# Kernel tuning notes

Hardware: AMD Instinct MI355X
Metric: run time of the kernel (lower is better)

The kernel has to match this reference:

```python
import jax, jax.numpy as jnp
import numpy as np
import math

D_MODEL = 1024
N_HEADS = 16
D_K = D_MODEL // N_HEADS
WIDTH_MULTIPLIER = 1.0  # readout=False on all projections, so unused in math


def setup_inputs() -> dict:
    key = jax.random.key(0)
    kx, kq, kk, kv, ko = jax.random.split(key, 5)
    std = 1.0 / math.sqrt(D_MODEL)  # init_scale=1.0 / sqrt(in_features)
    x = jax.random.normal(kx, (2, 2048, D_MODEL), dtype=jnp.float32)
    # weights stored as (out_features, in_features), matching torch
    Wq = jax.random.normal(kq, (D_MODEL, D_MODEL), dtype=jnp.float32) * std
    Wk = jax.random.normal(kk, (D_MODEL, D_MODEL), dtype=jnp.float32) * std
    Wv = jax.random.normal(kv, (D_MODEL, D_MODEL), dtype=jnp.float32) * std
    Wo = jax.random.normal(ko, (D_MODEL, D_MODEL), dtype=jnp.float32) * std
    return {"x": x, "Wq": Wq, "Wk": Wk, "Wv": Wv, "Wo": Wo}


def reference(x, Wq, Wk, Wv, Wo):
    B, S, D = x.shape
    H, Dk = N_HEADS, D_K
    # muPLinear: x @ W.T (bias=False, readout=False)
    q = jnp.einsum('bsd,ed->bse', x, Wq).reshape(B, S, H, Dk).transpose(0, 2, 1, 3)
    k = jnp.einsum('bsd,ed->bse', x, Wk).reshape(B, S, H, Dk).transpose(0, 2, 1, 3)
    v = jnp.einsum('bsd,ed->bse', x, Wv).reshape(B, S, H, Dk).transpose(0, 2, 1, 3)
    # full [B,H,S,S] scores, scaled by 1/sqrt(d_k), softmax over keys
    scores = jnp.einsum('bhqd,bhkd->bhqk', q, k) / math.sqrt(Dk)
    attn = jax.nn.softmax(scores, axis=-1)
    out = jnp.einsum('bhqk,bhkd->bhqd', attn, v)
    out = out.transpose(0, 2, 1, 3).reshape(B, S, D)
    return jnp.einsum('bsd,ed->bse', out, Wo)
```

## Files before the change

kernel.cpp:

```cpp
#include <hip/hip_runtime.h>
#include <hip/hip_bf16.h>
#include <math.h>

#define D_MODEL 1024
#define N_HEADS 16
#define D_K     64
#define BATCH   2
#define SEQ     2048
#define M_TOTAL (BATCH * SEQ)

typedef __attribute__((ext_vector_type(8))) short short8;
typedef __attribute__((ext_vector_type(4))) float f32x4;
typedef __attribute__((ext_vector_type(16))) float f32x16;

__device__ __forceinline__ ushort f2bf(float f) {
    __hip_bfloat16 h = __float2bfloat16(f);
    union { __hip_bfloat16 h; ushort u; } c; c.h = h; return c.u;
}

__device__ __forceinline__ uint packbf(float a, float b) {
    return ((uint)f2bf(b) << 16) | (uint)f2bf(a);
}

__device__ __forceinline__ void gload_lds16(const void* g, void* l) {
    __builtin_amdgcn_global_load_lds(
        (const __attribute__((address_space(1))) void*)g,
        (__attribute__((address_space(3))) void*)l, 16, 0, 0);
}

__device__ __forceinline__ void plswap(uint& a, uint& b) {
    asm volatile("v_permlane32_swap_b32 %0, %1" : "+v"(a), "+v"(b));
}

__global__ __launch_bounds__(256) void cast_all(const float* __restrict__ x,
                                                const float* __restrict__ Wq,
                                                const float* __restrict__ Wk,
                                                const float* __restrict__ Wv,
                                                const float* __restrict__ Wo,
                                                ushort* __restrict__ xb,
                                                ushort* __restrict__ wqkv,
                                                ushort* __restrict__ wob)
{
    const int bi = blockIdx.x;
    const float* src; ushort* dst; int blk;
    const int NW = D_MODEL * D_MODEL;
    if (bi < 4096)      { src = x;  dst = xb;            blk = bi; }
    else if (bi < 5120) { src = Wq; dst = wqkv;          blk = bi - 4096; }
    else if (bi < 6144) { src = Wk; dst = wqkv + NW;     blk = bi - 5120; }
    else if (bi < 7168) { src = Wv; dst = wqkv + 2 * NW; blk = bi - 6144; }
    else                { src = Wo; dst = wob;           blk = bi - 7168; }
    const int i = blk * 1024 + threadIdx.x * 4;
    float4 v = *(const float4*)&src[i];
    ushort4 o;
    o.x = f2bf(v.x); o.y = f2bf(v.y); o.z = f2bf(v.z); o.w = f2bf(v.w);
    *(ushort4*)&dst[i] = o;
}

template <int EPI>
__global__ __launch_bounds__(256) void gemm_bf16(const ushort* __restrict__ A,
                                                 const ushort* __restrict__ B,
                                                 void* __restrict__ C0,
                                                 void* __restrict__ C1,
                                                 void* __restrict__ C2,
                                                 int M, int N, int K)
{
    __shared__ ushort As[2][4 * 128 * 8];
    __shared__ ushort Bs[2][4 * 128 * 8];

    const int tid = threadIdx.x;
    const int lane = tid & 63;
    const int w = tid >> 6;
    const int li = lane & 15;
    const int kg = lane >> 4;
    const int m0 = blockIdx.y * 128;
    const int n0 = blockIdx.x * 128;
    const int wr = (w >> 1) * 64;
    const int wc = (w & 1) * 64;

    f32x4 acc[4][4] = {};

    const int s1 = tid, s2 = tid + 256;
    const ushort* ga1 = &A[(size_t)(m0 + (s1 & 127)) * K + (s1 >> 7) * 8];
    const ushort* ga2 = &A[(size_t)(m0 + (s2 & 127)) * K + (s2 >> 7) * 8];
    const ushort* gb1 = &B[(size_t)(n0 + (s1 & 127)) * K + (s1 >> 7) * 8];
    const ushort* gb2 = &B[(size_t)(n0 + (s2 & 127)) * K + (s2 >> 7) * 8];

    const int NT = K / 32;
    gload_lds16(ga1, &As[0][s1 * 8]);
    gload_lds16(ga2, &As[0][s2 * 8]);
    gload_lds16(gb1, &Bs[0][s1 * 8]);
    gload_lds16(gb2, &Bs[0][s2 * 8]);

    for (int t = 0; t < NT; ++t) {
        const int cur = t & 1;
        asm volatile("s_waitcnt vmcnt(0)" ::: "memory");
        __syncthreads();
        if (t + 1 < NT) {
            const int kb = (t + 1) * 32;
            const int nxt = cur ^ 1;
            gload_lds16(ga1 + kb, &As[nxt][s1 * 8]);
            gload_lds16(ga2 + kb, &As[nxt][s2 * 8]);
            gload_lds16(gb1 + kb, &Bs[nxt][s1 * 8]);
            gload_lds16(gb2 + kb, &Bs[nxt][s2 * 8]);
        }
        short8 af[4], bf_[4];
#pragma unroll
        for (int m = 0; m < 4; ++m)
            af[m] = *(const short8*)&As[cur][(kg * 128 + wr + m * 16 + li) * 8];
#pragma unroll
        for (int n = 0; n < 4; ++n)
            bf_[n] = *(const short8*)&Bs[cur][(kg * 128 + wc + n * 16 + li) * 8];
#pragma unroll
        for (int m = 0; m < 4; ++m)
#pragma unroll
            for (int n = 0; n < 4; ++n)
                acc[m][n] = __builtin_amdgcn_mfma_f32_16x16x32_bf16(
                    af[m], bf_[n], acc[m][n], 0, 0, 0);
    }

    if (EPI == 1) {
        ushort* q = (ushort*)C0; ushort* k = (ushort*)C1; ushort* v = (ushort*)C2;
        const float QSCALE = 0.125f * 1.44269504088896f;
#pragma unroll
        for (int m = 0; m < 4; ++m) {
            const int Rb = m0 + wr + m * 16 + kg * 4;
#pragma unroll
            for (int n = 0; n < 4; ++n) {
                const int Ncol = n0 + wc + n * 16 + li;
                const int proj = Ncol >> 10;
                const int rem = Ncol & 1023;
                const int h = rem >> 6, dk = rem & 63;
#pragma unroll
                for (int r = 0; r < 4; ++r) {
                    const int R = Rb + r;
                    const int b = R >> 11, s = R & 2047;
                    const int bh = b * N_HEADS + h;
                    if (proj == 0)
                        q[((size_t)bh * SEQ + s) * D_K + dk] = f2bf(acc[m][n][r] * QSCALE);
                    else if (proj == 1)
                        k[((size_t)bh * SEQ + s) * D_K + dk] = f2bf(acc[m][n][r]);
                    else
                        v[((size_t)bh * D_K + dk) * SEQ + s] = f2bf(acc[m][n][r]);
                }
            }
        }
    } else {
        float* C = (float*)C0;
#pragma unroll
        for (int m = 0; m < 4; ++m) {
            const int Rb = m0 + wr + m * 16 + kg * 4;
#pragma unroll
            for (int n = 0; n < 4; ++n) {
                const int Ncol = n0 + wc + n * 16 + li;
#pragma unroll
                for (int r = 0; r < 4; ++r)
                    C[(size_t)(Rb + r) * N + Ncol] = acc[m][n][r];
            }
        }
    }
}

__global__ __launch_bounds__(256) void attn_mfma(const ushort* __restrict__ Q,
                                                 const ushort* __restrict__ K,
                                                 const ushort* __restrict__ Vt,
                                                 ushort* __restrict__ AO)
{
    __shared__ ushort Ks[2][64 * 64];
    __shared__ ushort Vs[2][64 * 64];

    const int tid = threadIdx.x, lane = tid & 63, w = tid >> 6;
    const int r31 = lane & 31, hi = lane >> 5;
    const int b = blockIdx.z, h = blockIdx.y, q0 = blockIdx.x * 128;
    const int bh = b * N_HEADS + h;
    const size_t base = (size_t)bh * SEQ * D_K;
    const size_t vbase = (size_t)bh * D_K * SEQ;

    uint pa = (uint)lane, pbv = 1000u + (uint)lane;
    plswap(pa, pbv);
    const bool swap_lo = (__builtin_amdgcn_readfirstlane(pa) > 500u);

    const size_t qrow = base + (size_t)(q0 + w * 32 + r31) * D_K;
    short8 qb[4];
#pragma unroll
    for (int ks = 0; ks < 4; ++ks)
        qb[ks] = *(const short8*)&Q[qrow + ks * 16 + hi * 8];

    float m_ = -INFINITY, l_ = 0.f;
    f32x16 o0 = {}, o1 = {};

    const int srow_l = lane >> 3;
    const int sblk = lane & 7;
    const ushort* Kt0 = &K[base];
    const ushort* Vt0 = &Vt[vbase];

#define STAGE(kt_, buf_)                                                      \
    {                                                                         \
        _Pragma("unroll")                                                     \
        for (int p = 0; p < 2; ++p) {                                         \
            const int row = w * 16 + p * 8 + srow_l;                          \
            const int db = sblk ^ (row & 7);                                  \
            gload_lds16(Kt0 + ((size_t)((kt_) * 64 + row)) * D_K + db * 8,    \
                        &Ks[buf_][(w * 16 + p * 8) * 64]);                    \
            gload_lds16(Vt0 + (size_t)row * SEQ + (kt_) * 64 + db * 8,        \
                        &Vs[buf_][(w * 16 + p * 8) * 64]);                    \
        }                                                                     \
    }

    STAGE(0, 0);

    const int NT = SEQ / 64;
    for (int kt = 0; kt < NT; ++kt) {
        const int cur = kt & 1;
        asm volatile("s_waitcnt vmcnt(0)" ::: "memory");
        __syncthreads();
        if (kt + 1 < NT) STAGE(kt + 1, cur ^ 1);

        f32x16 s0 = {}, s1 = {};
#pragma unroll
        for (int ks = 0; ks < 4; ++ks) {
            const int row = r31;
            short8 kb = *(const short8*)&Ks[cur][row * 64 + (((2 * ks + hi) ^ (row & 7)) * 8)];
            s0 = __builtin_amdgcn_mfma_f32_32x32x16_bf16(kb, qb[ks], s0, 0, 0, 0);
        }
#pragma unroll
        for (int ks = 0; ks < 4; ++ks) {
            const int row = 32 + r31;
            short8 kb = *(const short8*)&Ks[cur][row * 64 + (((2 * ks + hi) ^ (row & 7)) * 8)];
            s1 = __builtin_amdgcn_mfma_f32_32x32x16_bf16(kb, qb[ks], s1, 0, 0, 0);
        }

        float mx = fmaxf(s0[0], s0[1]);
#pragma unroll
        for (int e = 2; e < 16; ++e) mx = fmaxf(mx, s0[e]);
#pragma unroll
        for (int e = 0; e < 16; ++e) mx = fmaxf(mx, s1[e]);
        mx = fmaxf(mx, __shfl_xor(mx, 32, 64));

        if (__any(mx > m_ + 8.0f)) {
            const float mn = fmaxf(m_, mx);
            const float sc = exp2f(m_ - mn);
            l_ *= sc;
#pragma unroll
            for (int e = 0; e < 16; ++e) { o0[e] *= sc; o1[e] *= sc; }
            m_ = mn;
        }

        f32x16 p0, p1;
        float ts = 0.f;
#pragma unroll
        for (int e = 0; e < 16; ++e) { p0[e] = exp2f(s0[e] - m_); ts += p0[e]; }
#pragma unroll
        for (int e = 0; e < 16; ++e) { p1[e] = exp2f(s1[e] - m_); ts += p1[e]; }
        ts += __shfl_xor(ts, 32, 64);
        l_ += ts;

        uint u[8][2];
#pragma unroll
        for (int rq = 0; rq < 4; ++rq) {
            u[rq][0]     = packbf(p0[4 * rq + 0], p0[4 * rq + 1]);
            u[rq][1]     = packbf(p0[4 * rq + 2], p0[4 * rq + 3]);
            u[4 + rq][0] = packbf(p1[4 * rq + 0], p1[4 * rq + 1]);
            u[4 + rq][1] = packbf(p1[4 * rq + 2], p1[4 * rq + 3]);
        }

        short8 pb[4];
#pragma unroll
        for (int ks = 0; ks < 4; ++ks) {
            uint x0 = u[2 * ks][0], x1 = u[2 * ks][1];
            uint y0 = u[2 * ks + 1][0], y1 = u[2 * ks + 1][1];
            if (swap_lo) { plswap(y0, x0); plswap(y1, x1); }
            else         { plswap(x0, y0); plswap(x1, y1); }
            union { uint u4[4]; short8 s; } pu;
            pu.u4[0] = x0; pu.u4[1] = x1; pu.u4[2] = y0; pu.u4[3] = y1;
            pb[ks] = pu.s;
        }

#pragma unroll
        for (int ks = 0; ks < 4; ++ks) {
            const int row = r31;
            short8 vb = *(const short8*)&Vs[cur][row * 64 + (((2 * ks + hi) ^ (row & 7)) * 8)];
            o0 = __builtin_amdgcn_mfma_f32_32x32x16_bf16(vb, pb[ks], o0, 0, 0, 0);
        }
#pragma unroll
        for (int ks = 0; ks < 4; ++ks) {
            const int row = 32 + r31;
            short8 vb = *(const short8*)&Vs[cur][row * 64 + (((2 * ks + hi) ^ (row & 7)) * 8)];
            o1 = __builtin_amdgcn_mfma_f32_32x32x16_bf16(vb, pb[ks], o1, 0, 0, 0);
        }
    }
#undef STAGE

    const float inv = 1.0f / l_;
    ushort* Ao = &AO[((size_t)b * SEQ + q0 + w * 32 + r31) * D_MODEL + h * 64];
#pragma unroll
    for (int rq = 0; rq < 4; ++rq) {
        uint2 v0, v1;
        v0.x = packbf(o0[4 * rq + 0] * inv, o0[4 * rq + 1] * inv);
        v0.y = packbf(o0[4 * rq + 2] * inv, o0[4 * rq + 3] * inv);
        v1.x = packbf(o1[4 * rq + 0] * inv, o1[4 * rq + 1] * inv);
        v1.y = packbf(o1[4 * rq + 2] * inv, o1[4 * rq + 3] * inv);
        *(uint2*)&Ao[8 * rq + 4 * hi]      = v0;
        *(uint2*)&Ao[32 + 8 * rq + 4 * hi] = v1;
    }
}

extern "C" void kernel_launch(void* const* d_in, const int* in_sizes, int n_in,
                              void* d_out, int out_size, void* d_ws, size_t ws_size,
                              hipStream_t stream)
{
    const float* x  = (const float*)d_in[0];
    const float* Wq = (const float*)d_in[1];
    const float* Wk = (const float*)d_in[2];
    const float* Wv = (const float*)d_in[3];
    const float* Wo = (const float*)d_in[4];
    float* out = (float*)d_out;

    ushort* xb   = (ushort*)d_ws;
    ushort* Wqkv = xb + (size_t)M_TOTAL * D_MODEL;
    ushort* Wob  = Wqkv + (size_t)3 * D_MODEL * D_MODEL;
    ushort* q    = Wob + (size_t)D_MODEL * D_MODEL;
    ushort* k    = q + (size_t)M_TOTAL * D_MODEL;
    ushort* vt   = k + (size_t)M_TOTAL * D_MODEL;
    ushort* ao   = vt + (size_t)M_TOTAL * D_MODEL;

    hipLaunchKernelGGL(cast_all, dim3(8192), dim3(256), 0, stream,
                       x, Wq, Wk, Wv, Wo, xb, Wqkv, Wob);

    hipLaunchKernelGGL((gemm_bf16<1>), dim3(3 * D_MODEL / 128, M_TOTAL / 128), dim3(256),
                       0, stream, xb, Wqkv, q, k, vt, M_TOTAL, 3 * D_MODEL, D_MODEL);

    hipLaunchKernelGGL(attn_mfma, dim3(SEQ / 128, N_HEADS, BATCH), dim3(256),
                       0, stream, q, k, vt, ao);

    hipLaunchKernelGGL((gemm_bf16<0>), dim3(D_MODEL / 128, M_TOTAL / 128), dim3(256),
                       0, stream, ao, Wob, out, (void*)0, (void*)0,
                       M_TOTAL, D_MODEL, D_MODEL);
}
```

Baseline: 187.5 us.

## Split attention KV range across two wave groups per block and merge in LDS

The attention block now has 512 threads. Two groups of four waves each process half of the key/value sequence for the same 128 query rows, each group with its own double-buffered LDS tiles. The partial softmax states (m, l, O) are then merged through shared memory before the output is written. The change also precomputes the swizzled LDS offsets, wraps the MFMA sections in s_setprio, and replaces the software bf16 packing with the v_cvt_pk_bf16_f32 instruction. The aim is to double the waves per tile and the memory-level parallelism, since the grid of 512 blocks would otherwise leave the GPU underfilled, at the cost of more LDS and an extra merge step.

```diff
diff --git a/kernel.cpp b/kernel.cpp
--- a/kernel.cpp
+++ b/kernel.cpp
@@ -20,6 +20,12 @@
 
 __device__ __forceinline__ uint packbf(float a, float b) {
     return ((uint)f2bf(b) << 16) | (uint)f2bf(a);
+}
+
+__device__ __forceinline__ uint cvtpk(float a, float b) {
+    uint r;
+    asm("v_cvt_pk_bf16_f32 %0, %1, %2" : "=v"(r) : "v"(a), "v"(b));
+    return r;
 }
 
 __device__ __forceinline__ void gload_lds16(const void* g, void* l) {
@@ -160,15 +166,15 @@
     }
 }
 
-__global__ __launch_bounds__(256) void attn_mfma(const ushort* __restrict__ Q,
-                                                 const ushort* __restrict__ K,
-                                                 const ushort* __restrict__ Vt,
-                                                 ushort* __restrict__ AO)
+__global__ __launch_bounds__(512, 4) void attn_mfma(const ushort* __restrict__ Q,
+                                                    const ushort* __restrict__ K,
+                                                    const ushort* __restrict__ Vt,
+                                                    ushort* __restrict__ AO)
 {
-    __shared__ ushort Ks[2][64 * 64];
-    __shared__ ushort Vs[2][64 * 64];
+    __shared__ ushort pool[2][2][2][64 * 64];
 
     const int tid = threadIdx.x, lane = tid & 63, w = tid >> 6;
+    const int wq = w & 3, kvh = w >> 2;
     const int r31 = lane & 31, hi = lane >> 5;
     const int b = blockIdx.z, h = blockIdx.y, q0 = blockIdx.x * 128;
     const int bh = b * N_HEADS + h;
@@ -179,7 +185,7 @@
     plswap(pa, pbv);
     const bool swap_lo = (__builtin_amdgcn_readfirstlane(pa) > 500u);
 
-    const size_t qrow = base + (size_t)(q0 + w * 32 + r31) * D_K;
+    const size_t qrow = base + (size_t)(q0 + wq * 32 + r31) * D_K;
     short8 qb[4];
 #pragma unroll
     for (int ks = 0; ks < 4; ++ks)
@@ -192,42 +198,55 @@
     const int sblk = lane & 7;
     const ushort* Kt0 = &K[base];
     const ushort* Vt0 = &Vt[vbase];
-
-#define STAGE(kt_, buf_)                                                      \
-    {                                                                         \
-        _Pragma("unroll")                                                     \
-        for (int p = 0; p < 2; ++p) {                                         \
-            const int row = w * 16 + p * 8 + srow_l;                          \
-            const int db = sblk ^ (row & 7);                                  \
-            gload_lds16(Kt0 + ((size_t)((kt_) * 64 + row)) * D_K + db * 8,    \
-                        &Ks[buf_][(w * 16 + p * 8) * 64]);                    \
-            gload_lds16(Vt0 + (size_t)row * SEQ + (kt_) * 64 + db * 8,        \
-                        &Vs[buf_][(w * 16 + p * 8) * 64]);                    \
-        }                                                                     \
+    const int tile0 = kvh * 16;
+
+    const int xr = r31 & 7;
+    int off[2][4];
+#pragma unroll
+    for (int hf = 0; hf < 2; ++hf)
+#pragma unroll
+        for (int ks = 0; ks < 4; ++ks)
+            off[hf][ks] = hf * 2048 + r31 * 64 + (((2 * ks + hi) ^ xr) * 8);
+
+    const ushort* Kst = &pool[kvh][0][0][0];
+    const ushort* Vst = &pool[kvh][1][0][0];
+
+#define STAGE(kt_, buf_)                                                       \
+    {                                                                          \
+        _Pragma("unroll")                                                      \
+        for (int p = 0; p < 2; ++p) {                                          \
+            const int row = wq * 16 + p * 8 + srow_l;                          \
+            const int db = sblk ^ (row & 7);                                   \
+            gload_lds16(Kt0 + ((size_t)((tile0 + (kt_)) * 64 + row)) * D_K + db * 8, \
+                        &pool[kvh][0][buf_][(wq * 16 + p * 8) * 64]);          \
+            gload_lds16(Vt0 + (size_t)row * SEQ + (tile0 + (kt_)) * 64 + db * 8,     \
+                        &pool[kvh][1][buf_][(wq * 16 + p * 8) * 64]);          \
+        }                                                                      \
     }
 
     STAGE(0, 0);
 
-    const int NT = SEQ / 64;
+    const int NT = SEQ / 64 / 2;
     for (int kt = 0; kt < NT; ++kt) {
         const int cur = kt & 1;
         asm volatile("s_waitcnt vmcnt(0)" ::: "memory");
         __syncthreads();
         if (kt + 1 < NT) STAGE(kt + 1, cur ^ 1);
+        const int cb = cur * 4096;
 
         f32x16 s0 = {}, s1 = {};
-#pragma unroll
-        for (int ks = 0; ks < 4; ++ks) {
-            const int row = r31;
-            short8 kb = *(const short8*)&Ks[cur][row * 64 + (((2 * ks + hi) ^ (row & 7)) * 8)];
+        __builtin_amdgcn_s_setprio(1);
+#pragma unroll
+        for (int ks = 0; ks < 4; ++ks) {
+            short8 kb = *(const short8*)(Kst + cb + off[0][ks]);
             s0 = __builtin_amdgcn_mfma_f32_32x32x16_bf16(kb, qb[ks], s0, 0, 0, 0);
         }
 #pragma unroll
         for (int ks = 0; ks < 4; ++ks) {
-            const int row = 32 + r31;
-            short8 kb = *(const short8*)&Ks[cur][row * 64 + (((2 * ks + hi) ^ (row & 7)) * 8)];
+            short8 kb = *(const short8*)(Kst + cb + off[1][ks]);
             s1 = __builtin_amdgcn_mfma_f32_32x32x16_bf16(kb, qb[ks], s1, 0, 0, 0);
         }
+        __builtin_amdgcn_s_setprio(0);
 
         float mx = fmaxf(s0[0], s0[1]);
 #pragma unroll
@@ -257,10 +276,10 @@
         uint u[8][2];
 #pragma unroll
         for (int rq = 0; rq < 4; ++rq) {
-            u[rq][0]     = packbf(p0[4 * rq + 0], p0[4 * rq + 1]);
-            u[rq][1]     = packbf(p0[4 * rq + 2], p0[4 * rq + 3]);
-            u[4 + rq][0] = packbf(p1[4 * rq + 0], p1[4 * rq + 1]);
-            u[4 + rq][1] = packbf(p1[4 * rq + 2], p1[4 * rq + 3]);
+            u[rq][0]     = cvtpk(p0[4 * rq + 0], p0[4 * rq + 1]);
+            u[rq][1]     = cvtpk(p0[4 * rq + 2], p0[4 * rq + 3]);
+            u[4 + rq][0] = cvtpk(p1[4 * rq + 0], p1[4 * rq + 1]);
+            u[4 + rq][1] = cvtpk(p1[4 * rq + 2], p1[4 * rq + 3]);
         }
 
         short8 pb[4];
@@ -275,32 +294,61 @@
             pb[ks] = pu.s;
         }
 
-#pragma unroll
-        for (int ks = 0; ks < 4; ++ks) {
-            const int row = r31;
-            short8 vb = *(const short8*)&Vs[cur][row * 64 + (((2 * ks + hi) ^ (row & 7)) * 8)];
+        __builtin_amdgcn_s_setprio(1);
+#pragma unroll
+        for (int ks = 0; ks < 4; ++ks) {
+            short8 vb = *(const short8*)(Vst + cb + off[0][ks]);
             o0 = __builtin_amdgcn_mfma_f32_32x32x16_bf16(vb, pb[ks], o0, 0, 0, 0);
         }
 #pragma unroll
         for (int ks = 0; ks < 4; ++ks) {
-            const int row = 32 + r31;
-            short8 vb = *(const short8*)&Vs[cur][row * 64 + (((2 * ks + hi) ^ (row & 7)) * 8)];
+            short8 vb = *(const short8*)(Vst + cb + off[1][ks]);
             o1 = __builtin_amdgcn_mfma_f32_32x32x16_bf16(vb, pb[ks], o1, 0, 0, 0);
         }
+        __builtin_amdgcn_s_setprio(0);
     }
 #undef STAGE
 
-    const float inv = 1.0f / l_;
-    ushort* Ao = &AO[((size_t)b * SEQ + q0 + w * 32 + r31) * D_MODEL + h * 64];
-#pragma unroll
-    for (int rq = 0; rq < 4; ++rq) {
-        uint2 v0, v1;
-        v0.x = packbf(o0[4 * rq + 0] * inv, o0[4 * rq + 1] * inv);
-        v0.y = packbf(o0[4 * rq + 2] * inv, o0[4 * rq + 3] * inv);
-        v1.x = packbf(o1[4 * rq + 0] * inv, o1[4 * rq + 1] * inv);
-        v1.y = packbf(o1[4 * rq + 2] * inv, o1[4 * rq + 3] * inv);
-        *(uint2*)&Ao[8 * rq + 4 * hi]      = v0;
-        *(uint2*)&Ao[32 + 8 * rq + 4 * hi] = v1;
+    __syncthreads();
+    float* cs = (float*)&pool[0][0][0][0];
+    float* ml = cs + 4 * 64 * 32;
+    const int cidx = (wq * 64 + lane) * 32;
+    if (kvh == 1) {
+#pragma unroll
+        for (int rq = 0; rq < 4; ++rq) {
+            f32x4 a, c;
+#pragma unroll
+            for (int e = 0; e < 4; ++e) { a[e] = o0[4 * rq + e]; c[e] = o1[4 * rq + e]; }
+            *(f32x4*)&cs[cidx + 4 * rq] = a;
+            *(f32x4*)&cs[cidx + 16 + 4 * rq] = c;
+        }
+        ml[(wq * 64 + lane) * 2]     = m_;
+        ml[(wq * 64 + lane) * 2 + 1] = l_;
+    }
+    __syncthreads();
+    if (kvh == 0) {
+        const float m2 = ml[(wq * 64 + lane) * 2];
+        const float l2 = ml[(wq * 64 + lane) * 2 + 1];
+        const float mM = fmaxf(m_, m2);
+        const float sc1 = exp2f(m_ - mM), sc2 = exp2f(m2 - mM);
+        const float linv = 1.f / (l_ * sc1 + l2 * sc2);
+        ushort* Ao = &AO[((size_t)b * SEQ + q0 + wq * 32 + r31) * D_MODEL + h * 64];
+#pragma unroll
+        for (int rq = 0; rq < 4; ++rq) {
+            f32x4 a = *(const f32x4*)&cs[cidx + 4 * rq];
+            f32x4 c = *(const f32x4*)&cs[cidx + 16 + 4 * rq];
+            uint2 v0, v1;
+            v0.x = cvtpk((o0[4 * rq + 0] * sc1 + a[0] * sc2) * linv,
+                         (o0[4 * rq + 1] * sc1 + a[1] * sc2) * linv);
+            v0.y = cvtpk((o0[4 * rq + 2] * sc1 + a[2] * sc2) * linv,
+                         (o0[4 * rq + 3] * sc1 + a[3] * sc2) * linv);
+            v1.x = cvtpk((o1[4 * rq + 0] * sc1 + c[0] * sc2) * linv,
+                         (o1[4 * rq + 1] * sc1 + c[1] * sc2) * linv);
+            v1.y = cvtpk((o1[4 * rq + 2] * sc1 + c[2] * sc2) * linv,
+                         (o1[4 * rq + 3] * sc1 + c[3] * sc2) * linv);
+            *(uint2*)&Ao[8 * rq + 4 * hi]      = v0;
+            *(uint2*)&Ao[32 + 8 * rq + 4 * hi] = v1;
+        }
     }
 }
 
@@ -329,7 +377,7 @@
     hipLaunchKernelGGL((gemm_bf16<1>), dim3(3 * D_MODEL / 128, M_TOTAL / 128), dim3(256),
                        0, stream, xb, Wqkv, q, k, vt, M_TOTAL, 3 * D_MODEL, D_MODEL);
 
-    hipLaunchKernelGGL(attn_mfma, dim3(SEQ / 128, N_HEADS, BATCH), dim3(256),
+    hipLaunchKernelGGL(attn_mfma, dim3(SEQ / 128, N_HEADS, BATCH), dim3(512),
                        0, stream, q, k, vt, ao);
 
     hipLaunchKernelGGL((gemm_bf16<0>), dim3(D_MODEL / 128, M_TOTAL / 128), dim3(256),
```

Measured after the change: 169.9 us. -9.4%, faster.
